# Optimization experiments

Measured on AMD Instinct MI355X. Metric: run time of the kernel, lower is better.

Reference implementation:

```python
import jax, jax.numpy as jnp
import numpy as np

B, NS, S, H = 512, 2, 128, 768
DS, NL = 384, 40
TEMP, ALPHA, GAMMA = 0.05, 0.15, 7.5
EPS = 1e-8


def setup_inputs() -> dict:
    key = jax.random.key(0)
    ks = jax.random.split(key, 8)
    return {
        "bert_emb": jax.random.normal(ks[0], (B, NS, S, H), dtype=jnp.float32),
        "rel_desc_emb": jax.random.normal(ks[1], (B, DS), dtype=jnp.float32),
        "dense_w": 0.02 * jax.random.normal(ks[2], (H, H), dtype=jnp.float32),
        "dense_b": jnp.zeros((H,), dtype=jnp.float32),
        "cls_w": 0.02 * jax.random.normal(ks[3], (3 * H, NL), dtype=jnp.float32),
        "cls_b": jnp.zeros((NL,), dtype=jnp.float32),
        "fc_w": 0.02 * jax.random.normal(ks[4], (3 * H, DS), dtype=jnp.float32),
        "fc_b": jnp.zeros((DS,), dtype=jnp.float32),
        "entity_idx": jax.random.randint(ks[5], (B, NS, 2), 0, S, dtype=jnp.int64 if jax.config.jax_enable_x64 else jnp.int32),
        "classify_labels": jax.random.randint(ks[6], (B,), 0, NL, dtype=jnp.int64 if jax.config.jax_enable_x64 else jnp.int32),
    }


def _mean_ce(logits, labels):
    lp = jax.nn.log_softmax(logits, axis=-1)
    return -jnp.mean(jnp.take_along_axis(lp, labels[:, None], axis=1))


def _l2n(x):
    return x / jnp.maximum(jnp.linalg.norm(x, axis=-1, keepdims=True), EPS)


def reference(bert_emb, rel_desc_emb, dense_w, dense_b, cls_w, cls_b, fc_w, fc_b,
              entity_idx, classify_labels):
    b = bert_emb.shape[0]
    bidx = jnp.arange(b)
    # ----- relation representation from sentence 0 (cls | head | tail) -----
    s0 = bert_emb[:, 0]                                   # [B,S,H]
    cls_tok = s0[:, 0]                                    # [B,H]
    head = s0[bidx, entity_idx[:, 0, 0]]                  # [B,H]
    tail = s0[bidx, entity_idx[:, 0, 1]]                  # [B,H]
    relation_hidden = jnp.tanh(jnp.concatenate([cls_tok, head, tail], axis=-1))  # [B,3H]
    logits = relation_hidden @ cls_w + cls_b              # [B,NL]
    ce_loss = _mean_ce(logits, classify_labels)
    # ----- margin loss vs relation-description embeddings (cosine) -----
    rel_emb = relation_hidden @ fc_w + fc_b               # [B,DS]
    C = _l2n(rel_emb) @ _l2n(rel_desc_emb).T              # [B,B] cosine sims
    pos = jnp.diagonal(C)
    diff_label = classify_labels[:, None] != classify_labels[None, :]
    neg = jnp.max(jnp.where(diff_label, C, -jnp.inf), axis=1)
    neg = jnp.maximum(neg, 0.0)                           # max_val initialized at 0
    margin_loss = jnp.sum(jax.nn.relu(neg - pos + GAMMA)) * (1.0 - ALPHA)
    ce_loss = ce_loss + margin_loss
    # ----- contrastive loss on (head|tail) entity pairs from both sents -----
    # dense is token-wise; apply only to the 4 gathered tokens per example
    h1a = bert_emb[bidx, 0, entity_idx[:, 0, 0]]
    h1b = bert_emb[bidx, 0, entity_idx[:, 0, 1]]
    h2a = bert_emb[bidx, 1, entity_idx[:, 1, 0]]
    h2b = bert_emb[bidx, 1, entity_idx[:, 1, 1]]
    toks = jnp.stack([h1a, h1b, h2a, h2b], axis=1)        # [B,4,H]
    toks = jnp.tanh(toks @ dense_w + dense_b)             # [B,4,H]
    z1 = toks[:, 0:2].reshape(b, -1)                      # [B,2H]
    z2 = toks[:, 2:4].reshape(b, -1)                      # [B,2H]
    cos_sim = (_l2n(z1) @ _l2n(z2).T) / TEMP              # [B,B]
    cl_loss = _mean_ce(cos_sim, bidx)
    return ce_loss + ALPHA * cl_loss
```

## Files before the change

### kernel.cpp

```cpp
#include <hip/hip_runtime.h>
#include <hip/hip_bf16.h>
#include <math.h>

#define B_   512
#define NS_  2
#define S_   128
#define H_   768
#define DS_  384
#define NL_  40
#define H3_  (3*H_)
#define TEMP_ 0.05f
#define ALPHA_ 0.15f
#define GAMMA_ 7.5f
#define EPS_ 1e-8f

typedef __attribute__((ext_vector_type(8))) short bf8_t;
typedef __attribute__((ext_vector_type(4))) short s4_t;
typedef __attribute__((ext_vector_type(4))) float f4_t;

#define LDSPAD 40


__device__ __forceinline__ short bfbits(float x) {
    __hip_bfloat16 h = __float2bfloat16(x);
    return *reinterpret_cast<short*>(&h);
}

__device__ __forceinline__ float block_reduce_sum(float v, float* sh) {
#pragma unroll
    for (int off = 32; off >= 1; off >>= 1) v += __shfl_down(v, off, 64);
    int w = threadIdx.x >> 6;
    if ((threadIdx.x & 63) == 0) sh[w] = v;
    __syncthreads();
    float r = (sh[0] + sh[1]) + (sh[2] + sh[3]);
    __syncthreads();
    return r;
}

__device__ __forceinline__ float block_reduce_max(float v, float* sh) {
#pragma unroll
    for (int off = 32; off >= 1; off >>= 1) v = fmaxf(v, __shfl_down(v, off, 64));
    int w = threadIdx.x >> 6;
    if ((threadIdx.x & 63) == 0) sh[w] = v;
    __syncthreads();
    float r = fmaxf(fmaxf(sh[0], sh[1]), fmaxf(sh[2], sh[3]));
    __syncthreads();
    return r;
}

__device__ __forceinline__ void transpose_tile(
    const float* __restrict__ in, __hip_bfloat16* __restrict__ out,
    int K, int N, int kt, int nt, int tid, float* tileLds )
{
    int k0 = kt * 32, n0 = nt * 32;
    int tx = tid & 31, ty = tid >> 5;
#pragma unroll
    for (int i = 0; i < 4; ++i) {
        int k = k0 + ty + i * 8, n = n0 + tx;
        if (k < K && n < N) tileLds[(ty + i*8) * 33 + tx] = in[(size_t)k * N + n];
    }
    __syncthreads();
#pragma unroll
    for (int i = 0; i < 4; ++i) {
        int n = n0 + ty + i * 8, k = k0 + tx;
        if (n < N && k < K) out[(size_t)n * K + k] = __float2bfloat16(tileLds[tx * 33 + ty + i*8]);
    }
}

__global__ __launch_bounds__(256) void prep_kernel(
    const float* __restrict__ bert, const int* __restrict__ eidx,
    const float* __restrict__ dense_w, const float* __restrict__ fc_w,
    const float* __restrict__ cls_w, const float* __restrict__ desc,
    __hip_bfloat16* __restrict__ rh_bf, __hip_bfloat16* __restrict__ toks_bf,
    __hip_bfloat16* __restrict__ dwt, __hip_bfloat16* __restrict__ fwt,
    __hip_bfloat16* __restrict__ cwt, __hip_bfloat16* __restrict__ desc_nb,
    float* __restrict__ acc, int* __restrict__ done)
{
    __shared__ float tileLds[32 * 33];
    int blk = blockIdx.x;
    int t = threadIdx.x;
    if (blk < 512) {
        int b = blk;
        if (b == 0) {
            if (t < 4) acc[t] = 0.0f;
            if (t == 4) *done = 0;
        }
        int e00 = eidx[b*4 + 0];
        int e01 = eidx[b*4 + 1];
        int e10 = eidx[b*4 + 2];
        int e11 = eidx[b*4 + 3];
        const float* s0 = bert + (size_t)b * NS_ * S_ * H_;
        const float* s1 = s0 + (size_t)S_ * H_;
        const float* cls  = s0;
        const float* head = s0 + (size_t)e00 * H_;
        const float* tail = s0 + (size_t)e01 * H_;
        const float* h2a  = s1 + (size_t)e10 * H_;
        const float* h2b  = s1 + (size_t)e11 * H_;
        __hip_bfloat16* rhb = rh_bf + (size_t)b * H3_;
        __hip_bfloat16* tk  = toks_bf + (size_t)b * 4 * H_;
        for (int h = t; h < H_; h += 256) {
            float c  = cls[h];
            float hd = head[h];
            float tl = tail[h];
            rhb[h]        = __float2bfloat16(tanhf(c));
            rhb[H_ + h]   = __float2bfloat16(tanhf(hd));
            rhb[2*H_ + h] = __float2bfloat16(tanhf(tl));
            tk[h]         = __float2bfloat16(hd);
            tk[H_ + h]    = __float2bfloat16(tl);
            tk[2*H_ + h]  = __float2bfloat16(h2a[h]);
            tk[3*H_ + h]  = __float2bfloat16(h2b[h]);
        }
    } else if (blk < 1088) {
        int q = blk - 512;
        transpose_tile(dense_w, dwt, H_, H_, q / 24, q % 24, t, tileLds);
    } else if (blk < 1952) {
        int q = blk - 1088;
        transpose_tile(fc_w, fwt, H3_, DS_, q / 12, q % 12, t, tileLds);
    } else if (blk < 2096) {
        int q = blk - 1952;
        int kt = q / 2, nt = q % 2;
        transpose_tile(cls_w, cwt, H3_, NL_, kt, nt, t, tileLds);
        if (nt == 1) {
            int tx = t & 31, ty = t >> 5;
            cwt[(size_t)(40 + ty) * H3_ + kt * 32 + tx] = __float2bfloat16(0.0f);
        }
    } else {
        int i = blk - 2096;
        const float* x = desc + (size_t)i * DS_;
        float ss = 0.0f;
        for (int d = t; d < DS_; d += 256) { float v = x[d]; ss += v * v; }
        ss = block_reduce_sum(ss, tileLds);
        float inv = 1.0f / fmaxf(sqrtf(ss), EPS_);
        __hip_bfloat16* o = desc_nb + (size_t)i * DS_;
        for (int d = t; d < DS_; d += 256) o[d] = __float2bfloat16(x[d] * inv);
    }
}


__device__ __forceinline__ void gemm128_body(
    const __hip_bfloat16* __restrict__ A, const __hip_bfloat16* __restrict__ Bp,
    const float* __restrict__ bias, float* __restrict__ C,
    int K, int lda, int ldb, int ldc, int fuse_tanh, int bx, int by,
    __hip_bfloat16* As0, __hip_bfloat16* Bs0,
    __hip_bfloat16* As1, __hip_bfloat16* Bs1)
{
    int tid  = threadIdx.x;
    int lane = tid & 63;
    int wave = tid >> 6;
    int wm = (wave >> 1) * 64;
    int wn = (wave & 1) * 64;
    int lr = lane & 15;
    int quad = lane >> 4;
    int rowBase = by * 128;
    int colBase = bx * 128;

    f4_t acc[4][4];
#pragma unroll
    for (int i = 0; i < 4; ++i)
#pragma unroll
        for (int j = 0; j < 4; ++j) acc[i][j] = (f4_t){0.f, 0.f, 0.f, 0.f};

    int sr = tid >> 2, sc = tid & 3;
    const __hip_bfloat16* Abase = A + (size_t)(rowBase + sr) * lda + sc * 8;
    const __hip_bfloat16* Bbase = Bp + (size_t)(colBase + sr) * ldb + sc * 8;
    size_t a64 = (size_t)64 * lda, b64 = (size_t)64 * ldb;

    *(bf8_t*)&As0[sr * LDSPAD + sc * 8]        = *(const bf8_t*)(Abase);
    *(bf8_t*)&As0[(sr + 64) * LDSPAD + sc * 8] = *(const bf8_t*)(Abase + a64);
    *(bf8_t*)&Bs0[sr * LDSPAD + sc * 8]        = *(const bf8_t*)(Bbase);
    *(bf8_t*)&Bs0[(sr + 64) * LDSPAD + sc * 8] = *(const bf8_t*)(Bbase + b64);
    __syncthreads();

    int nIter = K >> 5;
    for (int i = 0; i < nIter; ++i) {
        __hip_bfloat16* Asc = (i & 1) ? As1 : As0;
        __hip_bfloat16* Bsc = (i & 1) ? Bs1 : Bs0;
        __hip_bfloat16* Asn = (i & 1) ? As0 : As1;
        __hip_bfloat16* Bsn = (i & 1) ? Bs0 : Bs1;
        bf8_t pa0, pa1, pb0, pb1;
        bool pf = (i + 1 < nIter);
        if (pf) {
            int k = (i + 1) << 5;
            pa0 = *(const bf8_t*)(Abase + k);
            pa1 = *(const bf8_t*)(Abase + a64 + k);
            pb0 = *(const bf8_t*)(Bbase + k);
            pb1 = *(const bf8_t*)(Bbase + b64 + k);
        }
        bf8_t af[4], bfr[4];
#pragma unroll
        for (int f = 0; f < 4; ++f) {
            af[f]  = *(const bf8_t*)&Asc[(wm + f*16 + lr) * LDSPAD + quad * 8];
            bfr[f] = *(const bf8_t*)&Bsc[(wn + f*16 + lr) * LDSPAD + quad * 8];
        }
#pragma unroll
        for (int ii = 0; ii < 4; ++ii)
#pragma unroll
            for (int j = 0; j < 4; ++j)
                acc[ii][j] = __builtin_amdgcn_mfma_f32_16x16x32_bf16(af[ii], bfr[j], acc[ii][j], 0, 0, 0);
        if (pf) {
            *(bf8_t*)&Asn[sr * LDSPAD + sc * 8]        = pa0;
            *(bf8_t*)&Asn[(sr + 64) * LDSPAD + sc * 8] = pa1;
            *(bf8_t*)&Bsn[sr * LDSPAD + sc * 8]        = pb0;
            *(bf8_t*)&Bsn[(sr + 64) * LDSPAD + sc * 8] = pb1;
        }
        __syncthreads();
    }
#pragma unroll
    for (int j = 0; j < 4; ++j) {
        int col = colBase + wn + j*16 + lr;
        float bv = bias ? bias[col] : 0.0f;
#pragma unroll
        for (int i = 0; i < 4; ++i) {
            int row0 = rowBase + wm + i*16 + quad*4;
#pragma unroll
            for (int r = 0; r < 4; ++r) {
                float v = acc[i][j][r] + bv;
                if (fuse_tanh) v = tanhf(v);
                C[(size_t)(row0 + r) * ldc + col] = v;
            }
        }
    }
}

__device__ __forceinline__ void gemm64_body(
    const __hip_bfloat16* __restrict__ A, const __hip_bfloat16* __restrict__ Bp,
    float* __restrict__ C,
    int K, int kBase, int lda, int ldb, int ldc, float scale, int bx, int by,
    __hip_bfloat16* As0, __hip_bfloat16* Bs0,
    __hip_bfloat16* As1, __hip_bfloat16* Bs1)
{
    int tid  = threadIdx.x;
    int lane = tid & 63;
    int wave = tid >> 6;
    int lr = lane & 15;
    int quad = lane >> 4;
    int rowBase = by * 64;
    int colBase = bx * 64;

    f4_t acc[4];
#pragma unroll
    for (int i = 0; i < 4; ++i) acc[i] = (f4_t){0.f, 0.f, 0.f, 0.f};

    int sr = tid >> 2, sc = tid & 3;
    const __hip_bfloat16* Abase = A + (size_t)(rowBase + sr) * lda + kBase + sc * 8;
    const __hip_bfloat16* Bbase = Bp + (size_t)(colBase + sr) * ldb + kBase + sc * 8;

    *(bf8_t*)&As0[sr * LDSPAD + sc * 8] = *(const bf8_t*)(Abase);
    *(bf8_t*)&Bs0[sr * LDSPAD + sc * 8] = *(const bf8_t*)(Bbase);
    __syncthreads();

    int nIter = K >> 5;
    for (int i = 0; i < nIter; ++i) {
        __hip_bfloat16* Asc = (i & 1) ? As1 : As0;
        __hip_bfloat16* Bsc = (i & 1) ? Bs1 : Bs0;
        __hip_bfloat16* Asn = (i & 1) ? As0 : As1;
        __hip_bfloat16* Bsn = (i & 1) ? Bs0 : Bs1;
        bf8_t pa, pb;
        bool pf = (i + 1 < nIter);
        if (pf) {
            int k = (i + 1) << 5;
            pa = *(const bf8_t*)(Abase + k);
            pb = *(const bf8_t*)(Bbase + k);
        }
        bf8_t bfr = *(const bf8_t*)&Bsc[(wave*16 + lr) * LDSPAD + quad * 8];
#pragma unroll
        for (int f = 0; f < 4; ++f) {
            bf8_t af = *(const bf8_t*)&Asc[(f*16 + lr) * LDSPAD + quad * 8];
            acc[f] = __builtin_amdgcn_mfma_f32_16x16x32_bf16(af, bfr, acc[f], 0, 0, 0);
        }
        if (pf) {
            *(bf8_t*)&Asn[sr * LDSPAD + sc * 8] = pa;
            *(bf8_t*)&Bsn[sr * LDSPAD + sc * 8] = pb;
        }
        __syncthreads();
    }
    int col = colBase + wave*16 + lr;
#pragma unroll
    for (int f = 0; f < 4; ++f) {
        int row0 = rowBase + f*16 + quad*4;
#pragma unroll
        for (int r = 0; r < 4; ++r)
            C[(size_t)(row0 + r) * ldc + col] = acc[f][r] * scale;
    }
}

__device__ __forceinline__ void cls_ce_body(
    const __hip_bfloat16* __restrict__ rh, const __hip_bfloat16* __restrict__ cwt,
    const float* __restrict__ cls_b, const int* __restrict__ labels,
    float* __restrict__ acc, int rowBase, float* lgp )
{
    int tid  = threadIdx.x;
    int lane = tid & 63;
    int wave = tid >> 6;
    int lr = lane & 15;
    int quad = lane >> 4;

    f4_t a3[3];
#pragma unroll
    for (int j = 0; j < 3; ++j) a3[j] = (f4_t){0.f, 0.f, 0.f, 0.f};

    int kw0 = wave * (H3_ / 4);
    const __hip_bfloat16* aRow = rh + (size_t)(rowBase + lr) * H3_ + quad * 8;
#pragma unroll 2
    for (int s = 0; s < 18; ++s) {
        int k = kw0 + s * 32;
        bf8_t af = *(const bf8_t*)(aRow + k);
#pragma unroll
        for (int j = 0; j < 3; ++j) {
            bf8_t bfr = *(const bf8_t*)(cwt + (size_t)(j*16 + lr) * H3_ + k + quad * 8);
            a3[j] = __builtin_amdgcn_mfma_f32_16x16x32_bf16(af, bfr, a3[j], 0, 0, 0);
        }
    }
#pragma unroll
    for (int j = 0; j < 3; ++j) {
        int col = j*16 + lr;
#pragma unroll
        for (int r = 0; r < 4; ++r)
            lgp[wave * 768 + (quad*4 + r) * 48 + col] = a3[j][r];
    }
    __syncthreads();
    for (int idx = tid; idx < 768; idx += 256) {
        int col = idx % 48;
        float s = lgp[idx] + lgp[768 + idx] + lgp[1536 + idx] + lgp[2304 + idx];
        s = (col < NL_) ? (s + cls_b[col]) : -INFINITY;
        lgp[idx] = s;
    }
    __syncthreads();
    if (tid < 64) {
        float ce = 0.0f;
        if (tid < 16) {
            const float* Lr = &lgp[tid * 48];
            float m = -INFINITY;
            for (int c = 0; c < NL_; ++c) m = fmaxf(m, Lr[c]);
            float s = 0.0f;
            for (int c = 0; c < NL_; ++c) s += expf(Lr[c] - m);
            ce = logf(s) + m - Lr[labels[rowBase + tid]];
        }
        for (int off = 8; off >= 1; off >>= 1) ce += __shfl_down(ce, off);
        if (tid == 0) atomicAdd(acc + 0, ce * (1.0f / (float)B_));
    }
}

__global__ __launch_bounds__(256) void gemms_kernel(
    const __hip_bfloat16* __restrict__ toks_bf, const __hip_bfloat16* __restrict__ dwt,
    const float* __restrict__ dense_b, float* __restrict__ toks_out,
    const __hip_bfloat16* __restrict__ rh_bf, const __hip_bfloat16* __restrict__ fwt,
    float* __restrict__ relP0, float* __restrict__ relP1,
    const __hip_bfloat16* __restrict__ cwt, const float* __restrict__ cls_b,
    const int* __restrict__ labels, float* __restrict__ acc)
{
    __shared__ __align__(16) char smem[4 * 128 * LDSPAD * 2];
    __hip_bfloat16* s0 = (__hip_bfloat16*)smem;
    int blk = blockIdx.x;
    if (blk < 96) {
        gemm128_body(toks_bf, dwt, dense_b, toks_out, H_, H_, H_, H_, 1,
                     blk % 6, blk / 6,
                     s0, s0 + 128*LDSPAD, s0 + 2*128*LDSPAD, s0 + 3*128*LDSPAD);
    } else if (blk < 192) {
        int q = blk - 96;
        int half = q >= 48 ? 1 : 0;
        int q2 = q - 48 * half;
        gemm64_body(rh_bf, fwt, half ? relP1 : relP0, H3_/2, half * (H3_/2),
                    H3_, H3_, DS_, 1.0f, q2 % 6, q2 / 6,
                    s0, s0 + 64*LDSPAD, s0 + 2*64*LDSPAD, s0 + 3*64*LDSPAD);
    } else {
        cls_ce_body(rh_bf, cwt, cls_b, labels, acc, (blk - 192) * 16, (float*)smem);
    }
}

__global__ __launch_bounds__(256) void znorm_kernel(
    const float* __restrict__ relP0, const float* __restrict__ relP1,
    const float* __restrict__ fc_b, const float* __restrict__ toks_out,
    __hip_bfloat16* __restrict__ rel_nb, __hip_bfloat16* __restrict__ z_bf)
{
    __shared__ float sh[4];
    int blk = blockIdx.x, t = threadIdx.x;
    if (blk < 512) {
        const f4_t* p0 = (const f4_t*)(relP0 + (size_t)blk * DS_);
        const f4_t* p1 = (const f4_t*)(relP1 + (size_t)blk * DS_);
        const f4_t* bb = (const f4_t*)fc_b;
        f4_t v = (f4_t){0.f, 0.f, 0.f, 0.f};
        float ss = 0.0f;
        if (t < 96) {
            v = p0[t] + p1[t] + bb[t];
            ss = v[0]*v[0] + v[1]*v[1] + v[2]*v[2] + v[3]*v[3];
        }
        ss = block_reduce_sum(ss, sh);
        float inv = 1.0f / fmaxf(sqrtf(ss), EPS_);
        if (t < 96) {
            s4_t o = { bfbits(v[0]*inv), bfbits(v[1]*inv), bfbits(v[2]*inv), bfbits(v[3]*inv) };
            ((s4_t*)(rel_nb + (size_t)blk * DS_))[t] = o;
        }
    } else {
        int r = blk - 512;
        const f4_t* xv = (const f4_t*)(toks_out + (size_t)r * 2 * H_);
        f4_t v0 = xv[t];
        f4_t v1 = (t < 128) ? xv[256 + t] : (f4_t){0.f, 0.f, 0.f, 0.f};
        float ss = v0[0]*v0[0] + v0[1]*v0[1] + v0[2]*v0[2] + v0[3]*v0[3]
                 + v1[0]*v1[0] + v1[1]*v1[1] + v1[2]*v1[2] + v1[3]*v1[3];
        ss = block_reduce_sum(ss, sh);
        float inv = 1.0f / fmaxf(sqrtf(ss), EPS_);
        s4_t* ov = (s4_t*)(z_bf + (size_t)r * 2 * H_);
        s4_t o0 = { bfbits(v0[0]*inv), bfbits(v0[1]*inv), bfbits(v0[2]*inv), bfbits(v0[3]*inv) };
        ov[t] = o0;
        if (t < 128) {
            s4_t o1 = { bfbits(v1[0]*inv), bfbits(v1[1]*inv), bfbits(v1[2]*inv), bfbits(v1[3]*inv) };
            ov[256 + t] = o1;
        }
    }
}

__global__ __launch_bounds__(256) void c1c2_kernel(
    const __hip_bfloat16* __restrict__ rel_nb, const __hip_bfloat16* __restrict__ desc_nb,
    const __hip_bfloat16* __restrict__ z_bf,
    float* __restrict__ C1, float* __restrict__ C2a, float* __restrict__ C2b)
{
    __shared__ __align__(16) char smem[4 * 64 * LDSPAD * 2];
    __hip_bfloat16* s0 = (__hip_bfloat16*)smem;
    __hip_bfloat16* As0 = s0;
    __hip_bfloat16* Bs0 = s0 + 64*LDSPAD;
    __hip_bfloat16* As1 = s0 + 2*64*LDSPAD;
    __hip_bfloat16* Bs1 = s0 + 3*64*LDSPAD;
    int blk = blockIdx.x;
    if (blk < 64) {
        gemm64_body(rel_nb, desc_nb, C1, DS_, 0, DS_, DS_, B_, 1.0f,
                    blk % 8, blk / 8, As0, Bs0, As1, Bs1);
    } else {
        int q = blk - 64;
        int half = q >= 64 ? 1 : 0;
        int q2 = q - 64 * half;
        gemm64_body(z_bf, z_bf + 2*H_, half ? C2b : C2a, H_, half * H_,
                    4*H_, 4*H_, B_, 1.0f/TEMP_, q2 % 8, q2 / 8, As0, Bs0, As1, Bs1);
    }
}

__global__ __launch_bounds__(256) void tail_kernel(
    const float* __restrict__ C1, const float* __restrict__ C2a, const float* __restrict__ C2b,
    const int* __restrict__ labels, float* __restrict__ acc,
    int* __restrict__ done, float* __restrict__ out)
{
    __shared__ float sh[4];
    int blk = blockIdx.x, t = threadIdx.x;
    if (blk < 512) {
        int i = blk;
        int li = labels[i];
        const float* row = C1 + (size_t)i * B_;
        int j0 = t, j1 = t + 256;
        float m = -INFINITY;
        if (labels[j0] != li) m = row[j0];
        if (labels[j1] != li) m = fmaxf(m, row[j1]);
        float negmax = block_reduce_max(m, sh);
        if (t == 0) {
            float neg = fmaxf(negmax, 0.0f);
            float term = neg - row[i] + GAMMA_;
            if (term > 0.0f) atomicAdd(acc + 1, term);
        }
    } else {
        int i = blk - 512;
        const float* ra = C2a + (size_t)i * B_;
        const float* rb = C2b + (size_t)i * B_;
        int j0 = t, j1 = t + 256;
        float va = ra[j0] + rb[j0];
        float vb = ra[j1] + rb[j1];
        float m = block_reduce_max(fmaxf(va, vb), sh);
        float s = expf(va - m) + expf(vb - m);
        s = block_reduce_sum(s, sh);
        if (t == 0) {
            float pos = ra[i] + rb[i];
            atomicAdd(acc + 2, (logf(s) + m - pos) * (1.0f / (float)B_));
        }
    }
    __threadfence();
    if (t == 0) {
        int prev = atomicAdd(done, 1);
        if (prev == 1023) {
            float a0 = atomicAdd(acc + 0, 0.0f);
            float a1 = atomicAdd(acc + 1, 0.0f);
            float a2 = atomicAdd(acc + 2, 0.0f);
            out[0] = a0 + (1.0f - ALPHA_) * a1 + ALPHA_ * a2;
        }
    }
}


extern "C" void kernel_launch(void* const* d_in, const int* in_sizes, int n_in,
                              void* d_out, int out_size, void* d_ws, size_t ws_size,
                              hipStream_t stream) {
    const float* bert     = (const float*)d_in[0];
    const float* desc     = (const float*)d_in[1];
    const float* dense_w  = (const float*)d_in[2];
    const float* dense_b  = (const float*)d_in[3];
    const float* cls_w    = (const float*)d_in[4];
    const float* cls_b    = (const float*)d_in[5];
    const float* fc_w     = (const float*)d_in[6];
    const float* fc_b     = (const float*)d_in[7];
    const int*   eidx     = (const int*)d_in[8];
    const int*   labels   = (const int*)d_in[9];
    float* out = (float*)d_out;

    float* fp = (float*)d_ws;
    __hip_bfloat16* rh_bf   = (__hip_bfloat16*)fp; fp += (size_t)B_*H3_/2;
    __hip_bfloat16* toks_bf = (__hip_bfloat16*)fp; fp += (size_t)B_*4*H_/2;
    __hip_bfloat16* dwt_bf  = (__hip_bfloat16*)fp; fp += (size_t)H_*H_/2;
    __hip_bfloat16* fwt_bf  = (__hip_bfloat16*)fp; fp += (size_t)DS_*H3_/2;
    __hip_bfloat16* cwt_bf  = (__hip_bfloat16*)fp; fp += (size_t)48*H3_/2;
    __hip_bfloat16* desc_nb = (__hip_bfloat16*)fp; fp += (size_t)B_*DS_/2;
    __hip_bfloat16* rel_nb  = (__hip_bfloat16*)fp; fp += (size_t)B_*DS_/2;
    __hip_bfloat16* z_bf    = (__hip_bfloat16*)fp; fp += (size_t)B_*4*H_/2;
    float* toks_out = fp; fp += (size_t)B_*4*H_;
    float* relP0    = fp; fp += (size_t)B_*DS_;
    float* relP1    = fp; fp += (size_t)B_*DS_;
    float* C1       = fp; fp += (size_t)B_*B_;
    float* C2a      = fp; fp += (size_t)B_*B_;
    float* C2b      = fp; fp += (size_t)B_*B_;
    float* acc      = fp; fp += 4;
    int*   done     = (int*)fp;

    prep_kernel<<<2608, 256, 0, stream>>>(bert, eidx, dense_w, fc_w, cls_w, desc,
                                          rh_bf, toks_bf, dwt_bf, fwt_bf, cwt_bf,
                                          desc_nb, acc, done);

    gemms_kernel<<<224, 256, 0, stream>>>(toks_bf, dwt_bf, dense_b, toks_out,
                                          rh_bf, fwt_bf, relP0, relP1,
                                          cwt_bf, cls_b, labels, acc);

    znorm_kernel<<<1536, 256, 0, stream>>>(relP0, relP1, fc_b, toks_out, rel_nb, z_bf);

    c1c2_kernel<<<192, 256, 0, stream>>>(rel_nb, desc_nb, z_bf, C1, C2a, C2b);

    tail_kernel<<<1024, 256, 0, stream>>>(C1, C2a, C2b, labels, acc, done, out);
}
```

Before: 549.7 us.

## Fuse L2 normalization into dense GEMM epilogue and C1/C2 GEMMs, drop znorm kernel

Removes the separate znorm kernel. The dense GEMM epilogue now writes tanh outputs directly as bf16 and atomically accumulates per-token squared norms. The C2 GEMMs apply the inverse norms of both rows and columns in their epilogue. The C1 GEMM sums relP0+relP1+bias on load, converts to bf16 in LDS and accumulates row sums of squares, so it normalizes after the matmul rather than before. This saves one launch and the fp32 round trip of toks_out, at the cost of atomics and products computed from unnormalized bf16 values, which shifts rounding.

```diff
diff --git a/kernel.cpp b/kernel.cpp
--- a/kernel.cpp
+++ b/kernel.cpp
@@ -74,7 +74,7 @@
     __hip_bfloat16* __restrict__ rh_bf, __hip_bfloat16* __restrict__ toks_bf,
     __hip_bfloat16* __restrict__ dwt, __hip_bfloat16* __restrict__ fwt,
     __hip_bfloat16* __restrict__ cwt, __hip_bfloat16* __restrict__ desc_nb,
-    float* __restrict__ acc, int* __restrict__ done)
+    float* __restrict__ tok_ss, float* __restrict__ acc, int* __restrict__ done)
 {
     __shared__ float tileLds[32 * 33];
     int blk = blockIdx.x;
@@ -84,6 +84,9 @@
         if (b == 0) {
             if (t < 4) acc[t] = 0.0f;
             if (t == 4) *done = 0;
+        }
+        if (b == 1) {
+            for (int i = t; i < 4 * B_; i += 256) tok_ss[i] = 0.0f;
         }
         int e00 = eidx[b*4 + 0];
         int e01 = eidx[b*4 + 1];
@@ -136,11 +139,10 @@
     }
 }
 
-
-__device__ __forceinline__ void gemm128_body(
+__device__ __forceinline__ void dense128_body(
     const __hip_bfloat16* __restrict__ A, const __hip_bfloat16* __restrict__ Bp,
-    const float* __restrict__ bias, float* __restrict__ C,
-    int K, int lda, int ldb, int ldc, int fuse_tanh, int bx, int by,
+    const float* __restrict__ bias, __hip_bfloat16* __restrict__ Z,
+    float* __restrict__ tok_ss, int bx, int by,
     __hip_bfloat16* As0, __hip_bfloat16* Bs0,
     __hip_bfloat16* As1, __hip_bfloat16* Bs1)
 {
@@ -161,17 +163,17 @@
         for (int j = 0; j < 4; ++j) acc[i][j] = (f4_t){0.f, 0.f, 0.f, 0.f};
 
     int sr = tid >> 2, sc = tid & 3;
-    const __hip_bfloat16* Abase = A + (size_t)(rowBase + sr) * lda + sc * 8;
-    const __hip_bfloat16* Bbase = Bp + (size_t)(colBase + sr) * ldb + sc * 8;
-    size_t a64 = (size_t)64 * lda, b64 = (size_t)64 * ldb;
+    const __hip_bfloat16* Abase = A + (size_t)(rowBase + sr) * H_ + sc * 8;
+    const __hip_bfloat16* Bbase = Bp + (size_t)(colBase + sr) * H_ + sc * 8;
+    size_t a64 = (size_t)64 * H_;
 
     *(bf8_t*)&As0[sr * LDSPAD + sc * 8]        = *(const bf8_t*)(Abase);
     *(bf8_t*)&As0[(sr + 64) * LDSPAD + sc * 8] = *(const bf8_t*)(Abase + a64);
     *(bf8_t*)&Bs0[sr * LDSPAD + sc * 8]        = *(const bf8_t*)(Bbase);
-    *(bf8_t*)&Bs0[(sr + 64) * LDSPAD + sc * 8] = *(const bf8_t*)(Bbase + b64);
-    __syncthreads();
-
-    int nIter = K >> 5;
+    *(bf8_t*)&Bs0[(sr + 64) * LDSPAD + sc * 8] = *(const bf8_t*)(Bbase + a64);
+    __syncthreads();
+
+    const int nIter = H_ >> 5;
     for (int i = 0; i < nIter; ++i) {
         __hip_bfloat16* Asc = (i & 1) ? As1 : As0;
         __hip_bfloat16* Bsc = (i & 1) ? Bs1 : Bs0;
@@ -184,7 +186,7 @@
             pa0 = *(const bf8_t*)(Abase + k);
             pa1 = *(const bf8_t*)(Abase + a64 + k);
             pb0 = *(const bf8_t*)(Bbase + k);
-            pb1 = *(const bf8_t*)(Bbase + b64 + k);
+            pb1 = *(const bf8_t*)(Bbase + a64 + k);
         }
         bf8_t af[4], bfr[4];
 #pragma unroll
@@ -205,26 +207,39 @@
         }
         __syncthreads();
     }
-#pragma unroll
-    for (int j = 0; j < 4; ++j) {
-        int col = colBase + wn + j*16 + lr;
-        float bv = bias ? bias[col] : 0.0f;
-#pragma unroll
-        for (int i = 0; i < 4; ++i) {
-            int row0 = rowBase + wm + i*16 + quad*4;
-#pragma unroll
-            for (int r = 0; r < 4; ++r) {
-                float v = acc[i][j][r] + bv;
-                if (fuse_tanh) v = tanhf(v);
-                C[(size_t)(row0 + r) * ldc + col] = v;
+
+    float bv[4];
+#pragma unroll
+    for (int j = 0; j < 4; ++j) bv[j] = bias[colBase + wn + j*16 + lr];
+    float* rowp = (float*)As0;
+    int wnOff = wn ? 16 : 0;
+#pragma unroll
+    for (int i = 0; i < 4; ++i) {
+#pragma unroll
+        for (int r = 0; r < 4; ++r) {
+            int rowL = wm + i*16 + quad*4 + r;
+            float p = 0.0f;
+#pragma unroll
+            for (int j = 0; j < 4; ++j) {
+                float v = tanhf(acc[i][j][r] + bv[j]);
+                Z[(size_t)(rowBase + rowL) * H_ + colBase + wn + j*16 + lr] = __float2bfloat16(v);
+                p += v * v;
             }
-        }
+            rowp[rowL * 33 + wnOff + lr] = p;
+        }
+    }
+    __syncthreads();
+    if (tid < 128) {
+        float s = 0.0f;
+#pragma unroll
+        for (int k = 0; k < 32; ++k) s += rowp[tid * 33 + k];
+        atomicAdd(tok_ss + rowBase + tid, s);
     }
 }
 
 __device__ __forceinline__ void gemm64_body(
     const __hip_bfloat16* __restrict__ A, const __hip_bfloat16* __restrict__ Bp,
-    float* __restrict__ C,
+    float* __restrict__ C, const float* __restrict__ tok_ss,
     int K, int kBase, int lda, int ldb, int ldc, float scale, int bx, int by,
     __hip_bfloat16* As0, __hip_bfloat16* Bs0,
     __hip_bfloat16* As1, __hip_bfloat16* Bs1)
@@ -275,12 +290,107 @@
         __syncthreads();
     }
     int col = colBase + wave*16 + lr;
+    float cinv = 1.0f;
+    if (tok_ss) cinv = 1.0f / fmaxf(sqrtf(tok_ss[4*col + 2] + tok_ss[4*col + 3]), EPS_);
 #pragma unroll
     for (int f = 0; f < 4; ++f) {
-        int row0 = rowBase + f*16 + quad*4;
-#pragma unroll
-        for (int r = 0; r < 4; ++r)
-            C[(size_t)(row0 + r) * ldc + col] = acc[f][r] * scale;
+#pragma unroll
+        for (int r = 0; r < 4; ++r) {
+            int row = rowBase + f*16 + quad*4 + r;
+            float v = acc[f][r] * scale * cinv;
+            if (tok_ss) v *= 1.0f / fmaxf(sqrtf(tok_ss[4*row] + tok_ss[4*row + 1]), EPS_);
+            C[(size_t)row * ldc + col] = v;
+        }
+    }
+}
+
+__device__ __forceinline__ void c1_body(
+    const float* __restrict__ relP0, const float* __restrict__ relP1,
+    const float* __restrict__ fc_b, const __hip_bfloat16* __restrict__ descN,
+    float* __restrict__ C1, int bx, int by,
+    __hip_bfloat16* As0, __hip_bfloat16* Bs0,
+    __hip_bfloat16* As1, __hip_bfloat16* Bs1, float* rssLds )
+{
+    int tid  = threadIdx.x;
+    int lane = tid & 63;
+    int wave = tid >> 6;
+    int lr = lane & 15;
+    int quad = lane >> 4;
+    int rowBase = by * 64;
+    int colBase = bx * 64;
+
+    f4_t acc[4];
+#pragma unroll
+    for (int i = 0; i < 4; ++i) acc[i] = (f4_t){0.f, 0.f, 0.f, 0.f};
+
+    int sr = tid >> 2, sc = tid & 3;
+    const float* p0 = relP0 + (size_t)(rowBase + sr) * DS_ + sc * 8;
+    const float* p1 = relP1 + (size_t)(rowBase + sr) * DS_ + sc * 8;
+    const float* bb = fc_b + sc * 8;
+    const __hip_bfloat16* Bbase = descN + (size_t)(colBase + sr) * DS_ + sc * 8;
+    float rss = 0.0f;
+
+    {
+        f4_t u0 = *(const f4_t*)(p0);     f4_t u1 = *(const f4_t*)(p0 + 4);
+        f4_t w0 = *(const f4_t*)(p1);     f4_t w1 = *(const f4_t*)(p1 + 4);
+        f4_t b0 = *(const f4_t*)(bb);     f4_t b1 = *(const f4_t*)(bb + 4);
+        u0 += w0 + b0; u1 += w1 + b1;
+        rss += u0[0]*u0[0] + u0[1]*u0[1] + u0[2]*u0[2] + u0[3]*u0[3]
+             + u1[0]*u1[0] + u1[1]*u1[1] + u1[2]*u1[2] + u1[3]*u1[3];
+        s4_t o0 = { bfbits(u0[0]), bfbits(u0[1]), bfbits(u0[2]), bfbits(u0[3]) };
+        s4_t o1 = { bfbits(u1[0]), bfbits(u1[1]), bfbits(u1[2]), bfbits(u1[3]) };
+        *(s4_t*)&As0[sr * LDSPAD + sc * 8]     = o0;
+        *(s4_t*)&As0[sr * LDSPAD + sc * 8 + 4] = o1;
+        *(bf8_t*)&Bs0[sr * LDSPAD + sc * 8] = *(const bf8_t*)(Bbase);
+    }
+    __syncthreads();
+
+    const int nIter = DS_ >> 5;
+    for (int i = 0; i < nIter; ++i) {
+        __hip_bfloat16* Asc = (i & 1) ? As1 : As0;
+        __hip_bfloat16* Bsc = (i & 1) ? Bs1 : Bs0;
+        __hip_bfloat16* Asn = (i & 1) ? As0 : As1;
+        __hip_bfloat16* Bsn = (i & 1) ? Bs0 : Bs1;
+        bool pf = (i + 1 < nIter);
+        f4_t u0, u1, w0, w1, b0, b1; bf8_t pb;
+        if (pf) {
+            int k = (i + 1) << 5;
+            u0 = *(const f4_t*)(p0 + k);     u1 = *(const f4_t*)(p0 + k + 4);
+            w0 = *(const f4_t*)(p1 + k);     w1 = *(const f4_t*)(p1 + k + 4);
+            b0 = *(const f4_t*)(bb + k);     b1 = *(const f4_t*)(bb + k + 4);
+            pb = *(const bf8_t*)(Bbase + k);
+        }
+        bf8_t bfr = *(const bf8_t*)&Bsc[(wave*16 + lr) * LDSPAD + quad * 8];
+#pragma unroll
+        for (int f = 0; f < 4; ++f) {
+            bf8_t af = *(const bf8_t*)&Asc[(f*16 + lr) * LDSPAD + quad * 8];
+            acc[f] = __builtin_amdgcn_mfma_f32_16x16x32_bf16(af, bfr, acc[f], 0, 0, 0);
+        }
+        if (pf) {
+            u0 += w0 + b0; u1 += w1 + b1;
+            rss += u0[0]*u0[0] + u0[1]*u0[1] + u0[2]*u0[2] + u0[3]*u0[3]
+                 + u1[0]*u1[0] + u1[1]*u1[1] + u1[2]*u1[2] + u1[3]*u1[3];
+            s4_t o0 = { bfbits(u0[0]), bfbits(u0[1]), bfbits(u0[2]), bfbits(u0[3]) };
+            s4_t o1 = { bfbits(u1[0]), bfbits(u1[1]), bfbits(u1[2]), bfbits(u1[3]) };
+            *(s4_t*)&Asn[sr * LDSPAD + sc * 8]     = o0;
+            *(s4_t*)&Asn[sr * LDSPAD + sc * 8 + 4] = o1;
+            *(bf8_t*)&Bsn[sr * LDSPAD + sc * 8] = pb;
+        }
+        __syncthreads();
+    }
+
+    rssLds[sr * 4 + sc] = rss;
+    __syncthreads();
+    int col = colBase + wave*16 + lr;
+#pragma unroll
+    for (int f = 0; f < 4; ++f) {
+#pragma unroll
+        for (int r = 0; r < 4; ++r) {
+            int rowL = f*16 + quad*4 + r;
+            float ss = rssLds[rowL*4] + rssLds[rowL*4+1] + rssLds[rowL*4+2] + rssLds[rowL*4+3];
+            float inv = 1.0f / fmaxf(sqrtf(ss), EPS_);
+            C1[(size_t)(rowBase + rowL) * B_ + col] = acc[f][r] * inv;
+        }
     }
 }
 
@@ -343,7 +453,8 @@
 
 __global__ __launch_bounds__(256) void gemms_kernel(
     const __hip_bfloat16* __restrict__ toks_bf, const __hip_bfloat16* __restrict__ dwt,
-    const float* __restrict__ dense_b, float* __restrict__ toks_out,
+    const float* __restrict__ dense_b, __hip_bfloat16* __restrict__ z_bf,
+    float* __restrict__ tok_ss,
     const __hip_bfloat16* __restrict__ rh_bf, const __hip_bfloat16* __restrict__ fwt,
     float* __restrict__ relP0, float* __restrict__ relP1,
     const __hip_bfloat16* __restrict__ cwt, const float* __restrict__ cls_b,
@@ -353,83 +464,43 @@
     __hip_bfloat16* s0 = (__hip_bfloat16*)smem;
     int blk = blockIdx.x;
     if (blk < 96) {
-        gemm128_body(toks_bf, dwt, dense_b, toks_out, H_, H_, H_, H_, 1,
-                     blk % 6, blk / 6,
-                     s0, s0 + 128*LDSPAD, s0 + 2*128*LDSPAD, s0 + 3*128*LDSPAD);
+        dense128_body(toks_bf, dwt, dense_b, z_bf, tok_ss,
+                      blk % 6, blk / 6,
+                      s0, s0 + 128*LDSPAD, s0 + 2*128*LDSPAD, s0 + 3*128*LDSPAD);
     } else if (blk < 192) {
         int q = blk - 96;
         int half = q >= 48 ? 1 : 0;
         int q2 = q - 48 * half;
-        gemm64_body(rh_bf, fwt, half ? relP1 : relP0, H3_/2, half * (H3_/2),
-                    H3_, H3_, DS_, 1.0f, q2 % 6, q2 / 6,
+        gemm64_body(rh_bf, fwt, half ? relP1 : relP0, (const float*)nullptr,
+                    H3_/2, half * (H3_/2), H3_, H3_, DS_, 1.0f, q2 % 6, q2 / 6,
                     s0, s0 + 64*LDSPAD, s0 + 2*64*LDSPAD, s0 + 3*64*LDSPAD);
     } else {
         cls_ce_body(rh_bf, cwt, cls_b, labels, acc, (blk - 192) * 16, (float*)smem);
     }
 }
 
-__global__ __launch_bounds__(256) void znorm_kernel(
+__global__ __launch_bounds__(256) void c1c2_kernel(
     const float* __restrict__ relP0, const float* __restrict__ relP1,
-    const float* __restrict__ fc_b, const float* __restrict__ toks_out,
-    __hip_bfloat16* __restrict__ rel_nb, __hip_bfloat16* __restrict__ z_bf)
-{
-    __shared__ float sh[4];
-    int blk = blockIdx.x, t = threadIdx.x;
-    if (blk < 512) {
-        const f4_t* p0 = (const f4_t*)(relP0 + (size_t)blk * DS_);
-        const f4_t* p1 = (const f4_t*)(relP1 + (size_t)blk * DS_);
-        const f4_t* bb = (const f4_t*)fc_b;
-        f4_t v = (f4_t){0.f, 0.f, 0.f, 0.f};
-        float ss = 0.0f;
-        if (t < 96) {
-            v = p0[t] + p1[t] + bb[t];
-            ss = v[0]*v[0] + v[1]*v[1] + v[2]*v[2] + v[3]*v[3];
-        }
-        ss = block_reduce_sum(ss, sh);
-        float inv = 1.0f / fmaxf(sqrtf(ss), EPS_);
-        if (t < 96) {
-            s4_t o = { bfbits(v[0]*inv), bfbits(v[1]*inv), bfbits(v[2]*inv), bfbits(v[3]*inv) };
-            ((s4_t*)(rel_nb + (size_t)blk * DS_))[t] = o;
-        }
-    } else {
-        int r = blk - 512;
-        const f4_t* xv = (const f4_t*)(toks_out + (size_t)r * 2 * H_);
-        f4_t v0 = xv[t];
-        f4_t v1 = (t < 128) ? xv[256 + t] : (f4_t){0.f, 0.f, 0.f, 0.f};
-        float ss = v0[0]*v0[0] + v0[1]*v0[1] + v0[2]*v0[2] + v0[3]*v0[3]
-                 + v1[0]*v1[0] + v1[1]*v1[1] + v1[2]*v1[2] + v1[3]*v1[3];
-        ss = block_reduce_sum(ss, sh);
-        float inv = 1.0f / fmaxf(sqrtf(ss), EPS_);
-        s4_t* ov = (s4_t*)(z_bf + (size_t)r * 2 * H_);
-        s4_t o0 = { bfbits(v0[0]*inv), bfbits(v0[1]*inv), bfbits(v0[2]*inv), bfbits(v0[3]*inv) };
-        ov[t] = o0;
-        if (t < 128) {
-            s4_t o1 = { bfbits(v1[0]*inv), bfbits(v1[1]*inv), bfbits(v1[2]*inv), bfbits(v1[3]*inv) };
-            ov[256 + t] = o1;
-        }
-    }
-}
-
-__global__ __launch_bounds__(256) void c1c2_kernel(
-    const __hip_bfloat16* __restrict__ rel_nb, const __hip_bfloat16* __restrict__ desc_nb,
-    const __hip_bfloat16* __restrict__ z_bf,
+    const float* __restrict__ fc_b, const __hip_bfloat16* __restrict__ desc_nb,
+    const __hip_bfloat16* __restrict__ z_bf, const float* __restrict__ tok_ss,
     float* __restrict__ C1, float* __restrict__ C2a, float* __restrict__ C2b)
 {
-    __shared__ __align__(16) char smem[4 * 64 * LDSPAD * 2];
+    __shared__ __align__(16) char smem[4 * 64 * LDSPAD * 2 + 64 * 4 * 4];
     __hip_bfloat16* s0 = (__hip_bfloat16*)smem;
     __hip_bfloat16* As0 = s0;
     __hip_bfloat16* Bs0 = s0 + 64*LDSPAD;
     __hip_bfloat16* As1 = s0 + 2*64*LDSPAD;
     __hip_bfloat16* Bs1 = s0 + 3*64*LDSPAD;
+    float* rssLds = (float*)(smem + 4 * 64 * LDSPAD * 2);
     int blk = blockIdx.x;
     if (blk < 64) {
-        gemm64_body(rel_nb, desc_nb, C1, DS_, 0, DS_, DS_, B_, 1.0f,
-                    blk % 8, blk / 8, As0, Bs0, As1, Bs1);
+        c1_body(relP0, relP1, fc_b, desc_nb, C1, blk % 8, blk / 8,
+                As0, Bs0, As1, Bs1, rssLds);
     } else {
         int q = blk - 64;
         int half = q >= 64 ? 1 : 0;
         int q2 = q - 64 * half;
-        gemm64_body(z_bf, z_bf + 2*H_, half ? C2b : C2a, H_, half * H_,
+        gemm64_body(z_bf, z_bf + 2*H_, half ? C2b : C2a, tok_ss, H_, half * H_,
                     4*H_, 4*H_, B_, 1.0f/TEMP_, q2 % 8, q2 / 8, As0, Bs0, As1, Bs1);
     }
 }
@@ -505,28 +576,26 @@
     __hip_bfloat16* fwt_bf  = (__hip_bfloat16*)fp; fp += (size_t)DS_*H3_/2;
     __hip_bfloat16* cwt_bf  = (__hip_bfloat16*)fp; fp += (size_t)48*H3_/2;
     __hip_bfloat16* desc_nb = (__hip_bfloat16*)fp; fp += (size_t)B_*DS_/2;
-    __hip_bfloat16* rel_nb  = (__hip_bfloat16*)fp; fp += (size_t)B_*DS_/2;
     __hip_bfloat16* z_bf    = (__hip_bfloat16*)fp; fp += (size_t)B_*4*H_/2;
-    float* toks_out = fp; fp += (size_t)B_*4*H_;
     float* relP0    = fp; fp += (size_t)B_*DS_;
     float* relP1    = fp; fp += (size_t)B_*DS_;
     float* C1       = fp; fp += (size_t)B_*B_;
     float* C2a      = fp; fp += (size_t)B_*B_;
     float* C2b      = fp; fp += (size_t)B_*B_;
+    float* tok_ss   = fp; fp += (size_t)4*B_;
     float* acc      = fp; fp += 4;
     int*   done     = (int*)fp;
 
     prep_kernel<<<2608, 256, 0, stream>>>(bert, eidx, dense_w, fc_w, cls_w, desc,
                                           rh_bf, toks_bf, dwt_bf, fwt_bf, cwt_bf,
-                                          desc_nb, acc, done);
-
-    gemms_kernel<<<224, 256, 0, stream>>>(toks_bf, dwt_bf, dense_b, toks_out,
+                                          desc_nb, tok_ss, acc, done);
+
+    gemms_kernel<<<224, 256, 0, stream>>>(toks_bf, dwt_bf, dense_b, z_bf, tok_ss,
                                           rh_bf, fwt_bf, relP0, relP1,
                                           cwt_bf, cls_b, labels, acc);
 
-    znorm_kernel<<<1536, 256, 0, stream>>>(relP0, relP1, fc_b, toks_out, rel_nb, z_bf);
-
-    c1c2_kernel<<<192, 256, 0, stream>>>(rel_nb, desc_nb, z_bf, C1, C2a, C2b);
+    c1c2_kernel<<<192, 256, 0, stream>>>(relP0, relP1, fc_b, desc_nb,
+                                         z_bf, tok_ss, C1, C2a, C2b);
 
     tail_kernel<<<1024, 256, 0, stream>>>(C1, C2a, C2b, labels, acc, done, out);
 }
```

New measurement: 553.0 us. Within noise of the previous version (+0.6%).
